# Kernel tuning notes

Hardware: AMD Instinct MI355X
Metric: run time of the kernel (lower is better)

## Reference

```python
import math
import jax, jax.numpy as jnp
import numpy as np

NUM_POS_FEATS = 128
TEMPERATURE = 10000.0
NORMALIZE = True
SCALE = 2.0 * math.pi


def setup_inputs() -> dict:
    key = jax.random.key(0)
    x = jax.random.normal(key, (32, 256, 96, 96), dtype=jnp.float32)
    mask = jnp.zeros((32, 96, 96), dtype=jnp.bool_)  # all pixels valid
    return {"x": x, "mask": mask}


def reference(x, mask):
    F = NUM_POS_FEATS
    not_mask = ~mask
    # Running position indices along H (axis 1) and W (axis 2): [B,H,W]
    y_embed = jnp.cumsum(not_mask.astype(jnp.float32), axis=1)
    x_embed = jnp.cumsum(not_mask.astype(jnp.float32), axis=2)
    if NORMALIZE:
        eps = 1e-6
        y_embed = y_embed / (y_embed[:, -1:, :] + eps) * SCALE
        x_embed = x_embed / (x_embed[:, :, -1:] + eps) * SCALE
    k = jnp.arange(F)
    # dim_t[k] = temperature ** (2*(k//2)/F); even k -> sin, odd k -> cos
    inv_dim_t = TEMPERATURE ** (-2.0 * (k // 2).astype(jnp.float32) / F)  # [F]
    even = (k % 2 == 0)[None, :, None, None]                              # [1,F,1,1]
    ang_y = y_embed[:, None, :, :] * inv_dim_t[None, :, None, None]       # [B,F,H,W]
    ang_x = x_embed[:, None, :, :] * inv_dim_t[None, :, None, None]       # [B,F,H,W]
    pos_y = jnp.where(even, jnp.sin(ang_y), jnp.cos(ang_y))
    pos_x = jnp.where(even, jnp.sin(ang_x), jnp.cos(ang_x))
    return jnp.concatenate([pos_y, pos_x], axis=1).astype(x.dtype)  # [B,2F,H,W]
```

## Files before the change

kernel.cpp:

```cpp
#include <hip/hip_runtime.h>
#include <hip/hip_bf16.h>


#define BATCH 32
#define HH 96
#define WW 96
#define CC 256
#define F_HALF 128

#define LOG2_TEMP 13.287712379549449f
#define TWO_PI 6.2831853071795864769f

typedef float f32x4 __attribute__((ext_vector_type(4)));

__global__ void pes_cumsum_kernel(const unsigned char* __restrict__ mask,
                                  float* __restrict__ yemb,
                                  float* __restrict__ xemb) {
    int tid = blockIdx.x * blockDim.x + threadIdx.x;
    const float eps = 1e-6f;
    if (tid < BATCH * WW) {
        int b = tid / WW, w = tid % WW;
        const unsigned char* m = mask + (size_t)b * HH * WW + w;
        float* o = yemb + (size_t)b * HH * WW + w;
        float s = 0.f;
        for (int h = 0; h < HH; ++h) s += (m[h * WW] == 0) ? 1.f : 0.f;
        float f = TWO_PI / (s + eps);
        float cum = 0.f;
        for (int h = 0; h < HH; ++h) {
            cum += (m[h * WW] == 0) ? 1.f : 0.f;
            o[h * WW] = cum * f;
        }
    } else if (tid < 2 * BATCH * HH) {
        int t = tid - BATCH * WW;
        int b = t / HH, h = t % HH;
        const unsigned char* m = mask + ((size_t)b * HH + h) * WW;
        float* o = xemb + ((size_t)b * HH + h) * WW;
        float s = 0.f;
        for (int w = 0; w < WW; ++w) s += (m[w] == 0) ? 1.f : 0.f;
        float f = TWO_PI / (s + eps);
        float cum = 0.f;
        for (int w = 0; w < WW; ++w) {
            cum += (m[w] == 0) ? 1.f : 0.f;
            o[w] = cum * f;
        }
    }
}

#define PLANE   (HH * WW)
#define PLANE4  (PLANE / 4)
#define ITERS   (PLANE4 / 256)

__global__ void __launch_bounds__(256)
pes_gen_kernel(const float* __restrict__ yemb,
               const float* __restrict__ xemb,
               float* __restrict__ out) {
    int p = blockIdx.x;
    int b = p >> 7;
    int j = p & 127;

    int jj = j & 63;
    float inv = exp2f((float)jj * (-2.0f / (float)F_HALF) * LOG2_TEMP);

    const float* embbase = (j < 64) ? yemb : xemb;
    const f32x4* ep = (const f32x4*)(embbase + (size_t)b * PLANE);
    f32x4* op0 = (f32x4*)(out + ((size_t)b * CC + 2 * j) * PLANE);
    f32x4* op1 = op0 + PLANE4;

    int t = threadIdx.x;
#pragma unroll
    for (int it = 0; it < ITERS; ++it) {
        int idx = t + it * 256;
        f32x4 e = ep[idx];
        f32x4 a;
        a.x = e.x * inv; a.y = e.y * inv; a.z = e.z * inv; a.w = e.w * inv;
        f32x4 rs, rc;
        rs.x = __sinf(a.x); rs.y = __sinf(a.y); rs.z = __sinf(a.z); rs.w = __sinf(a.w);
        rc.x = __cosf(a.x); rc.y = __cosf(a.y); rc.z = __cosf(a.z); rc.w = __cosf(a.w);
        op0[idx] = rs;
        op1[idx] = rc;
    }
}

extern "C" void kernel_launch(void* const* d_in, const int* in_sizes, int n_in,
                              void* d_out, int out_size, void* d_ws, size_t ws_size,
                              hipStream_t stream) {
    const unsigned char* mask = (const unsigned char*)d_in[1];
    float* out = (float*)d_out;

    float* yemb = (float*)d_ws;
    float* xemb = yemb + (size_t)BATCH * PLANE;

    {
        int threads = 2 * BATCH * HH;
        int block = 256;
        int grid = (threads + block - 1) / block;
        pes_cumsum_kernel<<<grid, block, 0, stream>>>(mask, yemb, xemb);
    }

    pes_gen_kernel<<<BATCH * F_HALF, 256, 0, stream>>>(yemb, xemb, out);
}
```

Before: 61.00 us.

## Fuse cumsum into generator kernel, recomputing embeddings per block in LDS

Drops the separate cumsum kernel and its global workspace. Each generator block now recomputes its batch's y or x embedding plane from the mask into shared memory (padded pitch) and then computes sin/cos from LDS. This removes one kernel launch and the global round trip of the embedding planes. The cost is redundant mask scans (64 blocks per batch repeat the same work) and a serial 96-step prefix on at most 96 threads before a barrier, which delays the store phase.

```diff
diff --git a/kernel.cpp b/kernel.cpp
--- a/kernel.cpp
+++ b/kernel.cpp
@@ -7,70 +7,68 @@
 #define WW 96
 #define CC 256
 #define F_HALF 128
+#define PLANE   (HH * WW)
+#define PLANE4  (PLANE / 4)
+#define ITERS   (PLANE4 / 256)
+#define PITCH   100
 
 #define LOG2_TEMP 13.287712379549449f
 #define TWO_PI 6.2831853071795864769f
 
 typedef float f32x4 __attribute__((ext_vector_type(4)));
 
-__global__ void pes_cumsum_kernel(const unsigned char* __restrict__ mask,
-                                  float* __restrict__ yemb,
-                                  float* __restrict__ xemb) {
-    int tid = blockIdx.x * blockDim.x + threadIdx.x;
-    const float eps = 1e-6f;
-    if (tid < BATCH * WW) {
-        int b = tid / WW, w = tid % WW;
-        const unsigned char* m = mask + (size_t)b * HH * WW + w;
-        float* o = yemb + (size_t)b * HH * WW + w;
-        float s = 0.f;
-        for (int h = 0; h < HH; ++h) s += (m[h * WW] == 0) ? 1.f : 0.f;
-        float f = TWO_PI / (s + eps);
-        float cum = 0.f;
-        for (int h = 0; h < HH; ++h) {
-            cum += (m[h * WW] == 0) ? 1.f : 0.f;
-            o[h * WW] = cum * f;
-        }
-    } else if (tid < 2 * BATCH * HH) {
-        int t = tid - BATCH * WW;
-        int b = t / HH, h = t % HH;
-        const unsigned char* m = mask + ((size_t)b * HH + h) * WW;
-        float* o = xemb + ((size_t)b * HH + h) * WW;
-        float s = 0.f;
-        for (int w = 0; w < WW; ++w) s += (m[w] == 0) ? 1.f : 0.f;
-        float f = TWO_PI / (s + eps);
-        float cum = 0.f;
-        for (int w = 0; w < WW; ++w) {
-            cum += (m[w] == 0) ? 1.f : 0.f;
-            o[w] = cum * f;
-        }
-    }
-}
+__global__ void __launch_bounds__(256)
+pes_fused_kernel(const unsigned char* __restrict__ mask,
+                 float* __restrict__ out) {
+    __shared__ float emb[HH * PITCH];
 
-#define PLANE   (HH * WW)
-#define PLANE4  (PLANE / 4)
-#define ITERS   (PLANE4 / 256)
-
-__global__ void __launch_bounds__(256)
-pes_gen_kernel(const float* __restrict__ yemb,
-               const float* __restrict__ xemb,
-               float* __restrict__ out) {
     int p = blockIdx.x;
     int b = p >> 7;
     int j = p & 127;
+    int jj = j & 63;
 
-    int jj = j & 63;
     float inv = exp2f((float)jj * (-2.0f / (float)F_HALF) * LOG2_TEMP);
+    const unsigned char* mb = mask + (size_t)b * PLANE;
+    int t = threadIdx.x;
+    const float eps = 1e-6f;
 
-    const float* embbase = (j < 64) ? yemb : xemb;
-    const f32x4* ep = (const f32x4*)(embbase + (size_t)b * PLANE);
+    if (j < 64) {
+        if (t < WW) {
+            int w = t;
+            float s = 0.f;
+            for (int h = 0; h < HH; ++h) s += (mb[h * WW + w] == 0) ? 1.f : 0.f;
+            float f = TWO_PI / (s + eps);
+            float cum = 0.f;
+            for (int h = 0; h < HH; ++h) {
+                cum += (mb[h * WW + w] == 0) ? 1.f : 0.f;
+                emb[h * PITCH + w] = cum * f;
+            }
+        }
+    } else {
+        if (t < HH) {
+            int h = t;
+            const unsigned char* mr = mb + h * WW;
+            float s = 0.f;
+            for (int w = 0; w < WW; ++w) s += (mr[w] == 0) ? 1.f : 0.f;
+            float f = TWO_PI / (s + eps);
+            float cum = 0.f;
+            for (int w = 0; w < WW; ++w) {
+                cum += (mr[w] == 0) ? 1.f : 0.f;
+                emb[h * PITCH + w] = cum * f;
+            }
+        }
+    }
+    __syncthreads();
+
     f32x4* op0 = (f32x4*)(out + ((size_t)b * CC + 2 * j) * PLANE);
     f32x4* op1 = op0 + PLANE4;
 
-    int t = threadIdx.x;
 #pragma unroll
     for (int it = 0; it < ITERS; ++it) {
         int idx = t + it * 256;
-        f32x4 e = ep[idx];
+        int h = idx / 24;
+        int k = idx - h * 24;
+        f32x4 e = *(const f32x4*)&emb[h * PITCH + 4 * k];
         f32x4 a;
         a.x = e.x * inv; a.y = e.y * inv; a.z = e.z * inv; a.w = e.w * inv;
         f32x4 rs, rc;
@@ -87,15 +85,5 @@
     const unsigned char* mask = (const unsigned char*)d_in[1];
     float* out = (float*)d_out;
 
-    float* yemb = (float*)d_ws;
-    float* xemb = yemb + (size_t)BATCH * PLANE;
-
-    {
-        int threads = 2 * BATCH * HH;
-        int block = 256;
-        int grid = (threads + block - 1) / block;
-        pes_cumsum_kernel<<<grid, block, 0, stream>>>(mask, yemb, xemb);
-    }
-
-    pes_gen_kernel<<<BATCH * F_HALF, 256, 0, stream>>>(yemb, xemb, out);
+    pes_fused_kernel<<<BATCH * F_HALF, 256, 0, stream>>>(mask, out);
 }
```

After: 52.83 us. 1.15x faster.
